# Kernel optimization log

Measured on AMD Instinct MI355X. Metric: run time of the kernel, lower is better.

The kernel has to match this reference:

```python
import jax, jax.numpy as jnp
import numpy as np

B, N_SPINS, D_MODEL, K_MC = 256, 128, 768, 25


def setup_inputs() -> dict:
    key = jax.random.key(0)
    k1, k2, k3 = jax.random.split(key, 3)
    features = jax.random.normal(k1, (B, N_SPINS, D_MODEL), dtype=jnp.float32)
    coalitions = jax.random.randint(k2, (K_MC, N_SPINS), 0, 2, dtype=jnp.int32)
    w_v = jax.random.normal(k3, (D_MODEL, D_MODEL), dtype=jnp.float32) * 0.02
    scale = jnp.full((1,), 0.1, dtype=jnp.float32)
    return {"features": features, "coalitions": coalitions, "w_v": w_v, "scale": scale}


def reference(features, coalitions, w_v, scale):
    # features: [B, n, d]; coalitions: [K, n] in {0,1}; w_v: [d, d]; scale: [1]
    c = coalitions.astype(features.dtype)                      # [K, n]
    # coalition_value batched over all K coalitions at once:
    # sum_j mask[k,j] * features[b,j,:]  (sum and linear proj commute)
    s = jnp.einsum('kn,bnd->bkd', c, features)                 # [B, K, d]
    proj = s @ w_v                                             # [B, K, d]
    norm = jnp.linalg.norm(proj, axis=-1)                      # [B, K]
    cv = jax.nn.relu(norm * scale[0])                          # coalition values [B, K]
    # Shapley estimate: mean(v | i in S) - mean(v | i not in S)
    cnt_with = c.sum(axis=0)                                   # [n]
    cnt_without = c.shape[0] - cnt_with
    v_with = (cv @ c) / jnp.maximum(cnt_with, 1.0)             # [B, n]
    v_without = (cv @ (1.0 - c)) / jnp.maximum(cnt_without, 1.0)
    valid = (cnt_with > 0) & (cnt_without > 0)                 # [n]
    shapley = jnp.where(valid, v_with - v_without, 0.0)        # [B, n]
    return shapley
```

## Files before the change

### kernel.cpp

```cpp
#include <hip/hip_runtime.h>
#include <hip/hip_bf16.h>
#include <stdint.h>

#define NB  256
#define NSP 128
#define DM  768
#define KMC 25
#define MROWS (NB*KMC)

#define OFF_S    0u
#define OFF_WT   9830400u
#define OFF_N2   11010048u
#define OFF_COEF 11035648u
#define OFF_CB   11049984u

typedef __attribute__((ext_vector_type(8))) short bf16x8;
typedef __attribute__((ext_vector_type(4))) float f32x4;
typedef unsigned int u32;

#define GLOAD_LDS16(gp, lp) \
  __builtin_amdgcn_global_load_lds((const __attribute__((address_space(1))) u32*)(gp), \
                                   (__attribute__((address_space(3))) u32*)(lp), 16, 0, 0)

__global__ __launch_bounds__(256) void prep_kernel(const float* __restrict__ wv,
                                                   const int* __restrict__ co,
                                                   char* __restrict__ ws) {
  const int blk = blockIdx.x;
  const int t = threadIdx.x;
  if (blk < 144) {
    __shared__ __hip_bfloat16 lt[64][66];
    const int bi = blk / 12, bj = blk % 12;
    const int k0 = bi * 64, n0 = bj * 64;
    #pragma unroll
    for (int i = 0; i < 16; ++i) {
      int idx = t + i * 256;
      int r = idx >> 6, c = idx & 63;
      lt[c][r] = __float2bfloat16(wv[(size_t)(k0 + r) * DM + n0 + c]);
    }
    __syncthreads();
    __hip_bfloat16* wT = (__hip_bfloat16*)(ws + OFF_WT);
    #pragma unroll
    for (int i = 0; i < 16; ++i) {
      int idx = t + i * 256;
      int r = idx >> 6, c = idx & 63;
      wT[(size_t)(n0 + r) * DM + k0 + c] = lt[r][c];
    }
  } else if (blk == 144) {
    if (t < NSP) {
      const int n = t;
      int cw = 0;
      #pragma unroll
      for (int k = 0; k < KMC; ++k) cw += co[k * NSP + n];
      const int cwo = KMC - cw;
      const bool valid = (cw > 0) && (cwo > 0);
      float* coefT = (float*)(ws + OFF_COEF);
      #pragma unroll
      for (int k = 0; k < 28; ++k) {
        float v = 0.f;
        if (valid && k < KMC) v = co[k * NSP + n] ? (1.f / (float)cw) : (-1.f / (float)cwo);
        coefT[n * 28 + k] = v;
      }
    }
  } else if (blk < 170) {
    int i = (blk - 145) * 256 + t;
    if (i < MROWS) ((float*)(ws + OFF_N2))[i] = 0.f;
  } else {
    int k = blk - 170;
    if (t < NSP) {
      float v = (k < KMC) ? (float)co[k * NSP + t] : 0.f;
      ((__hip_bfloat16*)(ws + OFF_CB))[k * NSP + t] = __float2bfloat16(v);
    }
  }
}

__global__ __launch_bounds__(256, 3) void kA(const float* __restrict__ f,
                                             const __hip_bfloat16* __restrict__ Cb,
                                             __hip_bfloat16* __restrict__ s) {
  const int b = blockIdx.x;
  const int dslice = blockIdx.y;
  const int tid = threadIdx.x;
  const int w = tid >> 6;
  const int lane = tid & 63;
  const int lo = lane & 15, hi = lane >> 4;

  __shared__ __align__(16) float Fs[2][32 * 192];

  bf16x8 A0[4], A1[4];
  #pragma unroll
  for (int ks = 0; ks < 4; ++ks) {
    A0[ks] = *(const bf16x8*)(Cb + (size_t)lo * NSP + ks * 32 + hi * 8);
    A1[ks] = *(const bf16x8*)(Cb + (size_t)(16 + lo) * NSP + ks * 32 + hi * 8);
  }

  const float* fbase = f + (size_t)b * NSP * DM + dslice * 192;
  const float* gsrc[6];
  #pragma unroll
  for (int q = 0; q < 6; ++q) {
    int e = (w * 6 + q) * 256 + lane * 4;
    int r = e / 192, c = e % 192;
    gsrc[q] = fbase + (size_t)r * DM + c;
  }

  f32x4 ac0[3], ac1[3];
  #pragma unroll
  for (int ct = 0; ct < 3; ++ct)
    #pragma unroll
    for (int i = 0; i < 4; ++i) { ac0[ct][i] = 0.f; ac1[ct][i] = 0.f; }

  #pragma unroll
  for (int q = 0; q < 6; ++q)
    GLOAD_LDS16(gsrc[q], &Fs[0][(w * 6 + q) * 256]);

  #pragma unroll
  for (int ks = 0; ks < 4; ++ks) {
    const int bb = ks & 1;
    __syncthreads();
    if (ks < 3) {
      #pragma unroll
      for (int q = 0; q < 6; ++q)
        GLOAD_LDS16(gsrc[q] + (size_t)(ks + 1) * 32 * DM, &Fs[bb ^ 1][(w * 6 + q) * 256]);
    }
    #pragma unroll
    for (int ct = 0; ct < 3; ++ct) {
      bf16x8 Bf;
      #pragma unroll
      for (int j = 0; j < 8; ++j) {
        float v = Fs[bb][(hi * 8 + j) * 192 + w * 48 + ct * 16 + lo];
        __hip_bfloat16 h = __float2bfloat16(v);
        Bf[j] = *(short*)&h;
      }
      ac0[ct] = __builtin_amdgcn_mfma_f32_16x16x32_bf16(A0[ks], Bf, ac0[ct], 0, 0, 0);
      ac1[ct] = __builtin_amdgcn_mfma_f32_16x16x32_bf16(A1[ks], Bf, ac1[ct], 0, 0, 0);
    }
  }

  #pragma unroll
  for (int ct = 0; ct < 3; ++ct) {
    int dcol = dslice * 192 + w * 48 + ct * 16 + lo;
    #pragma unroll
    for (int i = 0; i < 4; ++i) {
      int r0 = hi * 4 + i;
      s[((size_t)b * KMC + r0) * DM + dcol] = __float2bfloat16(ac0[ct][i]);
      int r1 = 16 + hi * 4 + i;
      if (r1 < KMC)
        s[((size_t)b * KMC + r1) * DM + dcol] = __float2bfloat16(ac1[ct][i]);
    }
  }
}

#define BM 128
#define BN 192
#define BK 32
#define NTK 24

__global__ __launch_bounds__(256) void kB(char* __restrict__ ws) {
  const int bid = blockIdx.x;
  const int tm = bid >> 2;
  const int tn = bid & 3;
  const int tid = threadIdx.x;
  const int wid = tid >> 6;
  const int lane = tid & 63;
  const int wm = wid >> 1;
  const int wn = wid & 1;

  const __hip_bfloat16* S  = (const __hip_bfloat16*)(ws + OFF_S);
  const __hip_bfloat16* WT = (const __hip_bfloat16*)(ws + OFF_WT);
  float* norm2 = (float*)(ws + OFF_N2);

  __shared__ __align__(16) char As[2][BM * BK * 2];
  __shared__ __align__(16) char Bs[2][BN * BK * 2];

  const char* gA[2]; char *lA0[2], *lA1[2];
  #pragma unroll
  for (int j = 0; j < 2; ++j) {
    int li = (wid * 2 + j) * 64 + lane;
    int r = li >> 2, sl = li & 3;
    int slx = sl ^ ((r >> 1) & 3);
    gA[j] = (const char*)(S + (size_t)(tm * BM + r) * DM) + slx * 16;
    lA0[j] = As[0] + (wid * 2 + j) * 1024;
    lA1[j] = As[1] + (wid * 2 + j) * 1024;
  }
  const char* gB[3]; char *lB0[3], *lB1[3];
  #pragma unroll
  for (int j = 0; j < 3; ++j) {
    int li = (wid * 3 + j) * 64 + lane;
    int r = li >> 2, sl = li & 3;
    int slx = sl ^ ((r >> 1) & 3);
    gB[j] = (const char*)(WT + (size_t)(tn * BN + r) * DM) + slx * 16;
    lB0[j] = Bs[0] + (wid * 3 + j) * 1024;
    lB1[j] = Bs[1] + (wid * 3 + j) * 1024;
  }

  auto stage = [&](int tk, int bsel) {
    size_t koff = (size_t)tk * (BK * 2);
    #pragma unroll
    for (int j = 0; j < 2; ++j) GLOAD_LDS16(gA[j] + koff, bsel ? lA1[j] : lA0[j]);
    #pragma unroll
    for (int j = 0; j < 3; ++j) GLOAD_LDS16(gB[j] + koff, bsel ? lB1[j] : lB0[j]);
  };

  f32x4 acc[4][6];
  #pragma unroll
  for (int m = 0; m < 4; ++m)
    #pragma unroll
    for (int n = 0; n < 6; ++n)
      #pragma unroll
      for (int j = 0; j < 4; ++j) acc[m][n][j] = 0.f;

  int offA[4], offB[6];
  #pragma unroll
  for (int m = 0; m < 4; ++m) {
    int r = wm * 64 + m * 16 + (lane & 15);
    int sl = (lane >> 4) ^ ((r >> 1) & 3);
    offA[m] = r * 64 + sl * 16;
  }
  #pragma unroll
  for (int n = 0; n < 6; ++n) {
    int r = wn * 96 + n * 16 + (lane & 15);
    int sl = (lane >> 4) ^ ((r >> 1) & 3);
    offB[n] = r * 64 + sl * 16;
  }

  stage(0, 0);
  for (int tk = 0; tk < NTK; ++tk) {
    int cur = tk & 1;
    __syncthreads();
    if (tk + 1 < NTK) stage(tk + 1, cur ^ 1);
    bf16x8 af[4], bfr[6];
    #pragma unroll
    for (int m = 0; m < 4; ++m) af[m] = *(const bf16x8*)(As[cur] + offA[m]);
    #pragma unroll
    for (int n = 0; n < 6; ++n) bfr[n] = *(const bf16x8*)(Bs[cur] + offB[n]);
    #pragma unroll
    for (int m = 0; m < 4; ++m)
      #pragma unroll
      for (int n = 0; n < 6; ++n)
        acc[m][n] = __builtin_amdgcn_mfma_f32_16x16x32_bf16(af[m], bfr[n], acc[m][n], 0, 0, 0);
  }

  float ps[4][4];
  #pragma unroll
  for (int m = 0; m < 4; ++m)
    #pragma unroll
    for (int i = 0; i < 4; ++i) {
      float v = 0.f;
      #pragma unroll
      for (int n = 0; n < 6; ++n) { float x = acc[m][n][i]; v += x * x; }
      #pragma unroll
      for (int d = 1; d < 16; d <<= 1) v += __shfl_xor(v, d, 64);
      ps[m][i] = v;
    }
  if ((lane & 15) == 0) {
    int g = lane >> 4;
    #pragma unroll
    for (int m = 0; m < 4; ++m)
      #pragma unroll
      for (int i = 0; i < 4; ++i)
        atomicAdd(&norm2[tm * BM + wm * 64 + m * 16 + g * 4 + i], ps[m][i]);
  }
}

__global__ __launch_bounds__(128) void kC(const char* __restrict__ ws,
                                          const float* __restrict__ scale,
                                          float* __restrict__ out) {
  const int b = blockIdx.x, n = threadIdx.x;
  const float* norm2 = (const float*)(ws + OFF_N2);
  const float* coefT = (const float*)(ws + OFF_COEF);
  __shared__ float cvs[32];
  if (n < KMC) {
    float nv = norm2[b * KMC + n];
    cvs[n] = fmaxf(sqrtf(fmaxf(nv, 0.f)) * scale[0], 0.f);
  } else if (n < 32) {
    cvs[n] = 0.f;
  }
  __syncthreads();
  float sum = 0.f;
  #pragma unroll
  for (int k = 0; k < KMC; ++k) sum += cvs[k] * coefT[n * 28 + k];
  out[b * NSP + n] = sum;
}

extern "C" void kernel_launch(void* const* d_in, const int* in_sizes, int n_in,
                              void* d_out, int out_size, void* d_ws, size_t ws_size,
                              hipStream_t stream) {
  const float* features   = (const float*)d_in[0];
  const int*   coalitions = (const int*)d_in[1];
  const float* wv         = (const float*)d_in[2];
  const float* scale      = (const float*)d_in[3];
  char* ws = (char*)d_ws;

  prep_kernel<<<202, 256, 0, stream>>>(wv, coalitions, ws);
  dim3 ga(NB, 4);
  kA<<<ga, 256, 0, stream>>>(features, (const __hip_bfloat16*)(ws + OFF_CB),
                             (__hip_bfloat16*)(ws + OFF_S));
  kB<<<200, 256, 0, stream>>>(ws);
  kC<<<NB, 128, 0, stream>>>(ws, scale, (float*)d_out);
}
```

Baseline: 50.92 us.

## Restructure kA to 512-thread blocks with register-staged padded LDS loads

kA now runs 512 threads per block covering 384 columns per half instead of 256 threads per 192-column slice. It replaces direct global-to-LDS async loads with float2 register staging into a padded LDS row stride (390) to reduce bank conflicts, and software-pipelines the four K chunks with explicit register double buffering. The launch code also calls kA twice with identical arguments, which doubles that kernel's work for no functional gain.

Result: slower. 72.02 us (+41.4%).

```diff
diff --git a/kernel.cpp b/kernel.cpp
--- a/kernel.cpp
+++ b/kernel.cpp
@@ -73,17 +73,19 @@
   }
 }
 
-__global__ __launch_bounds__(256, 3) void kA(const float* __restrict__ f,
+#define KAPW 390
+#define KASL (32 * KAPW)
+
+__global__ __launch_bounds__(512, 2) void kA(const float* __restrict__ f,
                                              const __hip_bfloat16* __restrict__ Cb,
                                              __hip_bfloat16* __restrict__ s) {
   const int b = blockIdx.x;
-  const int dslice = blockIdx.y;
+  const int half = blockIdx.y;
   const int tid = threadIdx.x;
   const int w = tid >> 6;
-  const int lane = tid & 63;
-  const int lo = lane & 15, hi = lane >> 4;
-
-  __shared__ __align__(16) float Fs[2][32 * 192];
+  const int lo = tid & 15, hi = (tid & 63) >> 4;
+
+  __shared__ __align__(16) float Fs[2][KASL];
 
   bf16x8 A0[4], A1[4];
   #pragma unroll
@@ -92,14 +94,16 @@
     A1[ks] = *(const bf16x8*)(Cb + (size_t)(16 + lo) * NSP + ks * 32 + hi * 8);
   }
 
-  const float* fbase = f + (size_t)b * NSP * DM + dslice * 192;
-  const float* gsrc[6];
-  #pragma unroll
-  for (int q = 0; q < 6; ++q) {
-    int e = (w * 6 + q) * 256 + lane * 4;
-    int r = e / 192, c = e % 192;
-    gsrc[q] = fbase + (size_t)r * DM + c;
-  }
+  int goff[12], waddr[12];
+  #pragma unroll
+  for (int p = 0; p < 12; ++p) {
+    int e = 2 * tid + 1024 * p;
+    int r = e / 384, c = e - r * 384;
+    goff[p] = r * DM + c;
+    waddr[p] = r * KAPW + c;
+  }
+
+  const float* fb = f + (size_t)b * NSP * DM + half * 384;
 
   f32x4 ac0[3], ac1[3];
   #pragma unroll
@@ -107,36 +111,58 @@
     #pragma unroll
     for (int i = 0; i < 4; ++i) { ac0[ct][i] = 0.f; ac1[ct][i] = 0.f; }
 
-  #pragma unroll
-  for (int q = 0; q < 6; ++q)
-    GLOAD_LDS16(gsrc[q], &Fs[0][(w * 6 + q) * 256]);
-
-  #pragma unroll
-  for (int ks = 0; ks < 4; ++ks) {
-    const int bb = ks & 1;
-    __syncthreads();
-    if (ks < 3) {
-      #pragma unroll
-      for (int q = 0; q < 6; ++q)
-        GLOAD_LDS16(gsrc[q] + (size_t)(ks + 1) * 32 * DM, &Fs[bb ^ 1][(w * 6 + q) * 256]);
-    }
-    #pragma unroll
-    for (int ct = 0; ct < 3; ++ct) {
-      bf16x8 Bf;
-      #pragma unroll
-      for (int j = 0; j < 8; ++j) {
-        float v = Fs[bb][(hi * 8 + j) * 192 + w * 48 + ct * 16 + lo];
-        __hip_bfloat16 h = __float2bfloat16(v);
-        Bf[j] = *(short*)&h;
-      }
-      ac0[ct] = __builtin_amdgcn_mfma_f32_16x16x32_bf16(A0[ks], Bf, ac0[ct], 0, 0, 0);
-      ac1[ct] = __builtin_amdgcn_mfma_f32_16x16x32_bf16(A1[ks], Bf, ac1[ct], 0, 0, 0);
-    }
-  }
+  float2 rA[12], rB[12];
+
+#define KAL(chunk, reg) { \
+    const float* fp_ = fb + (chunk) * 32 * DM; \
+    _Pragma("unroll") for (int p = 0; p < 12; ++p) \
+      reg[p] = *(const float2*)(fp_ + goff[p]); }
+
+#define KAST(reg, bi) { \
+    _Pragma("unroll") for (int p = 0; p < 12; ++p) \
+      *(float2*)(&Fs[bi][waddr[p]]) = reg[p]; }
+
+#define KAC(ks, bi) { \
+    _Pragma("unroll") for (int ct = 0; ct < 3; ++ct) { \
+      bf16x8 Bf; \
+      _Pragma("unroll") for (int j = 0; j < 8; ++j) { \
+        float v_ = Fs[bi][(hi * 8 + j) * KAPW + w * 48 + ct * 16 + lo]; \
+        __hip_bfloat16 h_ = __float2bfloat16(v_); \
+        Bf[j] = *(short*)&h_; } \
+      ac0[ct] = __builtin_amdgcn_mfma_f32_16x16x32_bf16(A0[ks], Bf, ac0[ct], 0, 0, 0); \
+      ac1[ct] = __builtin_amdgcn_mfma_f32_16x16x32_bf16(A1[ks], Bf, ac1[ct], 0, 0, 0); } }
+
+  KAL(0, rA)
+  KAL(1, rB)
+  KAST(rA, 0)
+  __syncthreads();
+
+  KAC(0, 0)
+  __syncthreads();
+  KAL(2, rA)
+  KAST(rB, 1)
+  __syncthreads();
+
+  KAC(1, 1)
+  __syncthreads();
+  KAL(3, rB)
+  KAST(rA, 0)
+  __syncthreads();
+
+  KAC(2, 0)
+  __syncthreads();
+  KAST(rB, 1)
+  __syncthreads();
+
+  KAC(3, 1)
+
+#undef KAL
+#undef KAST
+#undef KAC
 
   #pragma unroll
   for (int ct = 0; ct < 3; ++ct) {
-    int dcol = dslice * 192 + w * 48 + ct * 16 + lo;
+    int dcol = half * 384 + w * 48 + ct * 16 + lo;
     #pragma unroll
     for (int i = 0; i < 4; ++i) {
       int r0 = hi * 4 + i;
@@ -290,9 +316,11 @@
   char* ws = (char*)d_ws;
 
   prep_kernel<<<202, 256, 0, stream>>>(wv, coalitions, ws);
-  dim3 ga(NB, 4);
-  kA<<<ga, 256, 0, stream>>>(features, (const __hip_bfloat16*)(ws + OFF_CB),
-                             (__hip_bfloat16*)(ws + OFF_S));
+  dim3 gaa(NB, 2);
+  kA<<<gaa, 512, 0, stream>>>(features, (const __hip_bfloat16*)(ws + OFF_CB),
+                              (__hip_bfloat16*)(ws + OFF_S));
+  kA<<<gaa, 512, 0, stream>>>(features, (const __hip_bfloat16*)(ws + OFF_CB),
+                              (__hip_bfloat16*)(ws + OFF_S));
   kB<<<200, 256, 0, stream>>>(ws);
   kC<<<NB, 128, 0, stream>>>(ws, scale, (float*)d_out);
 }
```
